# Kernel optimization log

Hardware: AMD Instinct MI355X
Metric: run time of the kernel (lower is better)

The kernel has to match this reference:

```python
import jax, jax.numpy as jnp
import numpy as np

H = 768          # hidden_size
NH = 12          # num heads
HD = H // NH     # head dim = 64
FF = 4 * H       # 3072
EPS = 1e-12


def _layer_norm(x, g, b):
    mu = jnp.mean(x, axis=-1, keepdims=True)
    var = jnp.var(x, axis=-1, keepdims=True)
    return (x - mu) * jax.lax.rsqrt(var + EPS) * g + b


def setup_inputs() -> dict:
    key = jax.random.key(0)
    ks = jax.random.split(key, 8)
    B, S = 4, 2048
    s = 0.02
    return {
        "x": jax.random.normal(ks[0], (B, S, H), dtype=jnp.float32),
        "w_qkv": jax.random.normal(ks[1], (H, 3 * H), dtype=jnp.float32) * s,
        "b_qkv": jnp.zeros((3 * H,), dtype=jnp.float32),
        "w_out": jax.random.normal(ks[2], (H, H), dtype=jnp.float32) * s,
        "b_out": jnp.zeros((H,), dtype=jnp.float32),
        "w_ff1": jax.random.normal(ks[3], (H, FF), dtype=jnp.float32) * s,
        "b_ff1": jnp.zeros((FF,), dtype=jnp.float32),
        "w_ff2": jax.random.normal(ks[4], (FF, H), dtype=jnp.float32) * s,
        "b_ff2": jnp.zeros((H,), dtype=jnp.float32),
        "g1": jnp.ones((H,), dtype=jnp.float32),
        "be1": jnp.zeros((H,), dtype=jnp.float32),
        "g2": jnp.ones((H,), dtype=jnp.float32),
        "be2": jnp.zeros((H,), dtype=jnp.float32),
    }


def reference(x, w_qkv, b_qkv, w_out, b_out, w_ff1, b_ff1, w_ff2, b_ff2, g1, be1, g2, be2):
    B, S, _ = x.shape
    qkv = x @ w_qkv + b_qkv                     # [B,S,3H]
    q, k, v = jnp.split(qkv, 3, axis=-1)
    # [B,S,H] -> [B,NH,S,HD]
    def heads(t):
        return t.reshape(B, S, NH, HD).transpose(0, 2, 1, 3)
    q, k, v = heads(q), heads(k), heads(v)
    scores = jnp.einsum("bhqd,bhkd->bhqk", q, k) / np.sqrt(HD).astype(np.float32)
    attn = jax.nn.softmax(scores, axis=-1)      # dropout is identity at inference
    ctx = jnp.einsum("bhqk,bhkd->bhqd", attn, v)
    ctx = ctx.transpose(0, 2, 1, 3).reshape(B, S, H)
    attn_out = ctx @ w_out + b_out
    x1 = _layer_norm(x + attn_out, g1, be1)
    h = jax.nn.gelu(x1 @ w_ff1 + b_ff1, approximate=False)  # torch exact gelu
    ffn = h @ w_ff2 + b_ff2
    return _layer_norm(x1 + ffn, g2, be2)
```

## Files before the change

### kernel.cpp

```cpp
#include <hip/hip_runtime.h>
#include <cstdint>
#include <cstddef>

typedef unsigned short u16;
typedef __attribute__((ext_vector_type(8))) short bf16x8;
typedef __attribute__((ext_vector_type(4))) float f32x4;
typedef __attribute__((ext_vector_type(16))) float f32x16;

__device__ __forceinline__ u16 f2b(float f) {
    union { float f; unsigned u; } un; un.f = f;
    unsigned r = un.u + 0x7fffu + ((un.u >> 16) & 1u);
    return (u16)(r >> 16);
}
__device__ __forceinline__ float b2f(u16 h) {
    union { unsigned u; float f; } un; un.u = ((unsigned)h) << 16;
    return un.f;
}
__device__ __forceinline__ float fast_exp2(float x) {
#if __has_builtin(__builtin_amdgcn_exp2f)
    return __builtin_amdgcn_exp2f(x);
#else
    return exp2f(x);
#endif
}
__device__ __forceinline__ float fast_rcp(float x) {
#if __has_builtin(__builtin_amdgcn_rcpf)
    return __builtin_amdgcn_rcpf(x);
#else
    return 1.f / x;
#endif
}
__device__ __forceinline__ float gelu_fast(float v) {
    const float s = fast_exp2(v * (2.30220842f + 0.10294324f * (v * v)));
    return v - v * fast_rcp(s + 1.f);
}

__device__ __forceinline__ void stage16(const u16* g, u16* l) {
    __builtin_amdgcn_global_load_lds(
        (const __attribute__((address_space(1))) void*)g,
        (__attribute__((address_space(3))) void*)l, 16, 0, 0);
}

__global__ __launch_bounds__(256)
void prep(const float* __restrict__ x, u16* __restrict__ xb,
          const float* __restrict__ wqkv, u16* __restrict__ wqkvT,
          const float* __restrict__ wout, u16* __restrict__ woutT,
          const float* __restrict__ wff1, u16* __restrict__ wff1T,
          const float* __restrict__ wff2, u16* __restrict__ wff2T) {
    __shared__ float t[32][33];
    const int tid = threadIdx.x;
    int bid = blockIdx.x;
    if (bid < 6144) {
        const int i = bid * 256 + tid;
        float4 v = ((const float4*)x)[i];
        ushort4 o;
        o.x = f2b(v.x); o.y = f2b(v.y); o.z = f2b(v.z); o.w = f2b(v.w);
        ((ushort4*)xb)[i] = o;
        return;
    }
    int tt = bid - 6144;
    const float* in; u16* out; int K, N, bx, by;
    if (tt < 1728)      { in = wqkv; out = wqkvT; K = 768;  N = 2304; bx = tt % 72; by = tt / 72; }
    else if ((tt -= 1728) < 576)  { in = wout; out = woutT; K = 768;  N = 768;  bx = tt % 24; by = tt / 24; }
    else if ((tt -= 576) < 2304)  { in = wff1; out = wff1T; K = 768;  N = 3072; bx = tt % 96; by = tt / 96; }
    else { tt -= 2304;    in = wff2; out = wff2T; K = 3072; N = 768;  bx = tt % 24; by = tt / 24; }
    const int n0 = bx * 32, k0 = by * 32;
    const int tx = tid & 31, ty = tid >> 5;
#pragma unroll
    for (int i = 0; i < 4; ++i)
        t[ty + i * 8][tx] = in[(size_t)(k0 + ty + i * 8) * N + n0 + tx];
    __syncthreads();
#pragma unroll
    for (int i = 0; i < 4; ++i)
        out[(size_t)(n0 + ty + i * 8) * K + k0 + tx] = f2b(t[tx][ty + i * 8]);
}

template <int EPI, int NTW>
__global__ __launch_bounds__(256, 3)
void gemm_bf16(const u16* __restrict__ A, const u16* __restrict__ BT,
               const float* __restrict__ bias,
               void* __restrict__ outp, u16* __restrict__ vt, int M, int N, int K) {
    __shared__ __align__(16) u16 Ash[128 * 64];
    __shared__ __align__(16) u16 Bsh[NTW * 64 * 64];
    const int m0 = blockIdx.y * 128, n0 = blockIdx.x * (NTW * 64);
    const int tid = threadIdx.x;
    const int w = tid >> 6, lane = tid & 63;
    const int l32 = lane & 31, half = lane >> 5;
    const int wm = (w >> 1) * 64, wn = (w & 1) * (NTW * 32);

    const int srow = lane >> 3;
    const int sgrp = (lane & 7) ^ (srow & 7);
    const int xr = l32 & 7;

    f32x16 acc[2][NTW];
#pragma unroll
    for (int i = 0; i < 2; ++i)
#pragma unroll
        for (int j = 0; j < NTW; ++j)
#pragma unroll
            for (int e = 0; e < 16; ++e) acc[i][j][e] = 0.f;

    for (int k0 = 0; k0 < K; k0 += 64) {
#pragma unroll
        for (int it = 0; it < 4; ++it) {
            const int c = it * 4 + w;
            const int r = c * 8 + srow;
            stage16(A + (size_t)(m0 + r) * K + k0 + sgrp * 8, &Ash[c * 512 + lane * 8]);
        }
#pragma unroll
        for (int it = 0; it < 2 * NTW; ++it) {
            const int c = it * 4 + w;
            const int r = c * 8 + srow;
            stage16(BT + (size_t)(n0 + r) * K + k0 + sgrp * 8, &Bsh[c * 512 + lane * 8]);
        }
        __syncthreads();

        if constexpr (NTW == 2) {
            bf16x8 af[2][4], bfr[2][4];
#pragma unroll
            for (int mt = 0; mt < 2; ++mt)
#pragma unroll
                for (int kc = 0; kc < 4; ++kc)
                    af[mt][kc] = *(const bf16x8*)&Ash[(wm + mt * 32 + l32) * 64 +
                                                      (((kc << 1) + half) ^ xr) * 8];
#pragma unroll
            for (int nt = 0; nt < 2; ++nt)
#pragma unroll
                for (int kc = 0; kc < 4; ++kc)
                    bfr[nt][kc] = *(const bf16x8*)&Bsh[(wn + nt * 32 + l32) * 64 +
                                                       (((kc << 1) + half) ^ xr) * 8];
#pragma unroll
            for (int mt = 0; mt < 2; ++mt)
#pragma unroll
                for (int nt = 0; nt < 2; ++nt)
#pragma unroll
                    for (int kc = 0; kc < 4; ++kc)
                        acc[mt][nt] = __builtin_amdgcn_mfma_f32_32x32x16_bf16(
                            af[mt][kc], bfr[nt][kc], acc[mt][nt], 0, 0, 0);
        } else {
#pragma unroll
            for (int kc = 0; kc < 4; ++kc) {
                const int ko = (((kc << 1) + half) ^ xr) * 8;
                bf16x8 a0 = *(const bf16x8*)&Ash[(wm + l32) * 64 + ko];
                bf16x8 a1 = *(const bf16x8*)&Ash[(wm + 32 + l32) * 64 + ko];
#pragma unroll
                for (int nt = 0; nt < NTW; ++nt) {
                    bf16x8 bv = *(const bf16x8*)&Bsh[(wn + nt * 32 + l32) * 64 + ko];
                    acc[0][nt] = __builtin_amdgcn_mfma_f32_32x32x16_bf16(
                        a0, bv, acc[0][nt], 0, 0, 0);
                    acc[1][nt] = __builtin_amdgcn_mfma_f32_32x32x16_bf16(
                        a1, bv, acc[1][nt], 0, 0, 0);
                }
            }
        }
        __syncthreads();
    }

    if (EPI == 3 && n0 >= 1536) {
#pragma unroll
        for (int mt = 0; mt < 2; ++mt) {
#pragma unroll
            for (int nt = 0; nt < NTW; ++nt) {
                const int col = n0 + wn + nt * 32 + l32;
                const int c = col - 1536;
                const int h = c >> 6, d = c & 63;
                const float bv = bias[col];
#pragma unroll
                for (int rq = 0; rq < 4; ++rq) {
                    const int row0 = m0 + wm + mt * 32 + rq * 8 + half * 4;
                    const int b = row0 >> 11, tok = row0 & 2047;
                    ushort4 o;
                    o.x = f2b(acc[mt][nt][rq * 4 + 0] + bv);
                    o.y = f2b(acc[mt][nt][rq * 4 + 1] + bv);
                    o.z = f2b(acc[mt][nt][rq * 4 + 2] + bv);
                    o.w = f2b(acc[mt][nt][rq * 4 + 3] + bv);
                    *(ushort4*)&vt[(size_t)(((b * 12 + h) << 6) + d) * 2048 + tok] = o;
                }
            }
        }
        return;
    }

#pragma unroll
    for (int mt = 0; mt < 2; ++mt) {
#pragma unroll
        for (int nt = 0; nt < NTW; ++nt) {
            const int col = n0 + wn + nt * 32 + l32;
            const float bv = bias[col];
#pragma unroll
            for (int reg = 0; reg < 16; ++reg) {
                const int row = m0 + wm + mt * 32 + (reg & 3) + 8 * (reg >> 2) + 4 * half;
                float v = acc[mt][nt][reg] + bv;
                if (EPI == 2)
                    v = gelu_fast(v);
                ((u16*)outp)[(size_t)row * N + col] = f2b(v);
            }
        }
    }
}

template <bool RESF32>
__global__ __launch_bounds__(256, 4)
void gemm_bf16_r64(const u16* __restrict__ A, const u16* __restrict__ BT,
                   const float* __restrict__ bias, const void* __restrict__ resid,
                   u16* __restrict__ outp, int M, int N, int K) {
    __shared__ __align__(16) u16 Ash[64 * 64];
    __shared__ __align__(16) u16 Bsh[128 * 64];
    const int m0 = blockIdx.y * 64, n0 = blockIdx.x * 128;
    const int tid = threadIdx.x;
    const int w = tid >> 6, lane = tid & 63;
    const int l32 = lane & 31, half = lane >> 5;
    const int wm = (w >> 1) * 32, wn = (w & 1) * 64;

    const int srow = lane >> 3;
    const int sgrp = (lane & 7) ^ (srow & 7);
    const int xr = l32 & 7;

    f32x16 acc[2];
#pragma unroll
    for (int j = 0; j < 2; ++j)
#pragma unroll
        for (int e = 0; e < 16; ++e) acc[j][e] = 0.f;

    for (int k0 = 0; k0 < K; k0 += 64) {
#pragma unroll
        for (int it = 0; it < 2; ++it) {
            const int c = it * 4 + w;
            const int r = c * 8 + srow;
            stage16(A + (size_t)(m0 + r) * K + k0 + sgrp * 8, &Ash[c * 512 + lane * 8]);
        }
#pragma unroll
        for (int it = 0; it < 4; ++it) {
            const int c = it * 4 + w;
            const int r = c * 8 + srow;
            stage16(BT + (size_t)(n0 + r) * K + k0 + sgrp * 8, &Bsh[c * 512 + lane * 8]);
        }
        __syncthreads();

        bf16x8 af[4], bfr[2][4];
#pragma unroll
        for (int kc = 0; kc < 4; ++kc)
            af[kc] = *(const bf16x8*)&Ash[(wm + l32) * 64 + (((kc << 1) + half) ^ xr) * 8];
#pragma unroll
        for (int nt = 0; nt < 2; ++nt)
#pragma unroll
            for (int kc = 0; kc < 4; ++kc)
                bfr[nt][kc] = *(const bf16x8*)&Bsh[(wn + nt * 32 + l32) * 64 +
                                                   (((kc << 1) + half) ^ xr) * 8];
#pragma unroll
        for (int nt = 0; nt < 2; ++nt)
#pragma unroll
            for (int kc = 0; kc < 4; ++kc)
                acc[nt] = __builtin_amdgcn_mfma_f32_32x32x16_bf16(
                    af[kc], bfr[nt][kc], acc[nt], 0, 0, 0);
        __syncthreads();
    }

#pragma unroll
    for (int nt = 0; nt < 2; ++nt) {
        const int col = n0 + wn + nt * 32 + l32;
        const float bv = bias[col];
#pragma unroll
        for (int reg = 0; reg < 16; ++reg) {
            const int row = m0 + wm + (reg & 3) + 8 * (reg >> 2) + 4 * half;
            const size_t idx = (size_t)row * N + col;
            const float rv = RESF32 ? ((const float*)resid)[idx]
                                    : b2f(((const u16*)resid)[idx]);
            outp[idx] = f2b(acc[nt][reg] + bv + rv);
        }
    }
}

__global__ __launch_bounds__(256, 3)
void attn_fused(const u16* __restrict__ qkv, const u16* __restrict__ vt,
                u16* __restrict__ ctx) {
    __shared__ __align__(16) u16 Ksh[2][64 * 64];
    __shared__ __align__(16) u16 Vsh[2][64 * 64];

    const int orig = blockIdx.x;
    const int swz = (orig & 7) * 96 + (orig >> 3);
    const int q0 = (swz & 15) * 128;
    const int bh = swz >> 4;
    const int h = bh % 12, b = bh / 12;

    const int tid = threadIdx.x;
    const int w = tid >> 6, lane = tid & 63;
    const int l32 = lane & 31, hi5 = lane >> 5;
    const int xr8 = l32 & 7;

    const int srow = lane >> 3;
    const int sgrp = (lane & 7) ^ (srow & 7);

    const u16* Qp = qkv + (size_t)b * 2048 * 2304 + h * 64;
    const u16* Kp = Qp + 768;
    const u16* Vtp = vt + ((size_t)(b * 12 + h) << 6) * 2048;

    bf16x8 qf[4];
#pragma unroll
    for (int ks = 0; ks < 4; ++ks)
        qf[ks] = *(const bf16x8*)(Qp +
            (size_t)(q0 + w * 32 + l32) * 2304 + ks * 16 + hi5 * 8);
    asm volatile("s_waitcnt vmcnt(0)" ::: "memory");
    __builtin_amdgcn_sched_barrier(0);

    f32x16 oacc[2];
#pragma unroll
    for (int dt = 0; dt < 2; ++dt)
#pragma unroll
        for (int e = 0; e < 16; ++e) oacc[dt][e] = 0.f;
    float ls0 = 0.f, ls1 = 0.f, ls2 = 0.f, ls3 = 0.f;

    constexpr float SCALE = 0.18033688011112042f;

    auto stage_kv = [&](int buf, int ktt) {
#pragma unroll
        for (int it = 0; it < 2; ++it) {
            const int c = it * 4 + w;
            const int r = c * 8 + srow;
            stage16(Kp + (size_t)(ktt + r) * 2304 + sgrp * 8,
                    &Ksh[buf][c * 512 + lane * 8]);
        }
#pragma unroll
        for (int it = 0; it < 2; ++it) {
            const int c = it * 4 + w;
            const int r = c * 8 + srow;
            stage16(Vtp + (size_t)r * 2048 + ktt + sgrp * 8,
                    &Vsh[buf][c * 512 + lane * 8]);
        }
    };

    stage_kv(0, 0);

    for (int t = 0; t < 32; ++t) {
        const int cur = t & 1;
        if (t < 31) {
            stage_kv(cur ^ 1, (t + 1) * 64);
            asm volatile("s_waitcnt vmcnt(4)" ::: "memory");
        } else {
            asm volatile("s_waitcnt vmcnt(0)" ::: "memory");
        }
        __builtin_amdgcn_sched_barrier(0);
        __builtin_amdgcn_s_barrier();

        f32x16 sacc[2];
#pragma unroll
        for (int nt = 0; nt < 2; ++nt)
#pragma unroll
            for (int e = 0; e < 16; ++e) sacc[nt][e] = 0.f;

        __builtin_amdgcn_s_setprio(1);
#pragma unroll
        for (int nt = 0; nt < 2; ++nt)
#pragma unroll
            for (int ks = 0; ks < 4; ++ks) {
                bf16x8 kfr = *(const bf16x8*)&Ksh[cur][(nt * 32 + l32) * 64 +
                                                      (((ks << 1) + hi5) ^ xr8) * 8];
                sacc[nt] = __builtin_amdgcn_mfma_f32_32x32x16_bf16(
                    kfr, qf[ks], sacc[nt], 0, 0, 0);
            }
        __builtin_amdgcn_s_setprio(0);

#pragma unroll
        for (int nt = 0; nt < 2; ++nt) {
#pragma unroll
            for (int e = 0; e < 16; ++e)
                sacc[nt][e] = fast_exp2(sacc[nt][e] * SCALE);
            ls0 += sacc[nt][0] + sacc[nt][1];
            ls1 += sacc[nt][2] + sacc[nt][3];
            ls2 += sacc[nt][4] + sacc[nt][5];
            ls3 += sacc[nt][6] + sacc[nt][7];
            ls0 += sacc[nt][8] + sacc[nt][9];
            ls1 += sacc[nt][10] + sacc[nt][11];
            ls2 += sacc[nt][12] + sacc[nt][13];
            ls3 += sacc[nt][14] + sacc[nt][15];
        }

        __builtin_amdgcn_s_setprio(1);
#pragma unroll
        for (int nt = 0; nt < 2; ++nt) {
#pragma unroll
            for (int kh = 0; kh < 2; ++kh) {
                const int rb = kh * 8;
                unsigned c01, c23, c45, c67;
                asm("v_cvt_pk_bf16_f32 %0, %1, %2"
                    : "=v"(c01) : "v"(sacc[nt][rb + 0]), "v"(sacc[nt][rb + 1]));
                asm("v_cvt_pk_bf16_f32 %0, %1, %2"
                    : "=v"(c23) : "v"(sacc[nt][rb + 2]), "v"(sacc[nt][rb + 3]));
                asm("v_cvt_pk_bf16_f32 %0, %1, %2"
                    : "=v"(c45) : "v"(sacc[nt][rb + 4]), "v"(sacc[nt][rb + 5]));
                asm("v_cvt_pk_bf16_f32 %0, %1, %2"
                    : "=v"(c67) : "v"(sacc[nt][rb + 6]), "v"(sacc[nt][rb + 7]));
                asm("v_permlane32_swap_b32 %0, %1" : "+v"(c01), "+v"(c45));
                asm("v_permlane32_swap_b32 %0, %1" : "+v"(c23), "+v"(c67));
                union { unsigned u[4]; bf16x8 v; } pf;
                pf.u[0] = c01; pf.u[1] = c23; pf.u[2] = c45; pf.u[3] = c67;
#pragma unroll
                for (int dt = 0; dt < 2; ++dt) {
                    bf16x8 vfr = *(const bf16x8*)&Vsh[cur][(dt * 32 + l32) * 64 +
                        (((nt << 2) + (kh << 1) + hi5) ^ xr8) * 8];
                    oacc[dt] = __builtin_amdgcn_mfma_f32_32x32x16_bf16(
                        pf.v, vfr, oacc[dt], 0, 0, 0);
                }
            }
        }
        __builtin_amdgcn_s_setprio(0);
        __builtin_amdgcn_s_barrier();
    }

    float lsum = (ls0 + ls1) + (ls2 + ls3);
    lsum += __shfl_xor(lsum, 32);
    const float linv = 1.f / lsum;

    float scv[16];
#pragma unroll
    for (int reg = 0; reg < 16; ++reg) {
        const int q_r = (reg & 3) + 8 * (reg >> 2) + 4 * hi5;
        scv[reg] = __shfl(linv, q_r);
    }

#pragma unroll
    for (int dt = 0; dt < 2; ++dt)
#pragma unroll
        for (int reg = 0; reg < 16; ++reg) {
            const int q_r = (reg & 3) + 8 * (reg >> 2) + 4 * hi5;
            const int row = q0 + w * 32 + q_r;
            ctx[(size_t)(b * 2048 + row) * 768 + h * 64 + dt * 32 + l32] =
                f2b(oacc[dt][reg] * scv[reg]);
        }
}

template <bool OUTF32>
__global__ __launch_bounds__(256)
void layernorm_k(const u16* __restrict__ y, const float* __restrict__ g,
                 const float* __restrict__ be, float* __restrict__ outf,
                 u16* __restrict__ outb) {
    const int row = blockIdx.x;
    const int tid = threadIdx.x;
    const u16* yr = y + (size_t)row * 768;
    float v[3], s = 0.f, s2 = 0.f;
#pragma unroll
    for (int i = 0; i < 3; ++i) {
        float x = b2f(yr[tid + i * 256]);
        v[i] = x; s += x; s2 += x * x;
    }
#pragma unroll
    for (int off = 32; off >= 1; off >>= 1) {
        s += __shfl_xor(s, off);
        s2 += __shfl_xor(s2, off);
    }
    __shared__ float red[2][4];
    const int w = tid >> 6;
    if ((tid & 63) == 0) { red[0][w] = s; red[1][w] = s2; }
    __syncthreads();
    s = red[0][0] + red[0][1] + red[0][2] + red[0][3];
    s2 = red[1][0] + red[1][1] + red[1][2] + red[1][3];
    const float mu = s * (1.f / 768.f);
    const float var = s2 * (1.f / 768.f) - mu * mu;
    const float rs = rsqrtf(var + 1e-12f);
#pragma unroll
    for (int i = 0; i < 3; ++i) {
        const int c = tid + i * 256;
        const float o = (v[i] - mu) * rs * g[c] + be[c];
        if (OUTF32) outf[(size_t)row * 768 + c] = o;
        else        outb[(size_t)row * 768 + c] = f2b(o);
    }
}

extern "C" void kernel_launch(void* const* d_in, const int* in_sizes, int n_in,
                              void* d_out, int out_size, void* d_ws, size_t ws_size,
                              hipStream_t stream) {
    const float* x    = (const float*)d_in[0];
    const float* wqkv = (const float*)d_in[1];
    const float* bqkv = (const float*)d_in[2];
    const float* wout = (const float*)d_in[3];
    const float* bout = (const float*)d_in[4];
    const float* wff1 = (const float*)d_in[5];
    const float* bff1 = (const float*)d_in[6];
    const float* wff2 = (const float*)d_in[7];
    const float* bff2 = (const float*)d_in[8];
    const float* g1   = (const float*)d_in[9];
    const float* be1  = (const float*)d_in[10];
    const float* g2   = (const float*)d_in[11];
    const float* be2  = (const float*)d_in[12];

    char* ws = (char*)d_ws;
    constexpr size_t o_xb    = 0;
    constexpr size_t o_wqkvT = o_xb    + (size_t)8192 * 768 * 2;
    constexpr size_t o_woutT = o_wqkvT + (size_t)2304 * 768 * 2;
    constexpr size_t o_wff1T = o_woutT + (size_t)768 * 768 * 2;
    constexpr size_t o_wff2T = o_wff1T + (size_t)3072 * 768 * 2;
    constexpr size_t o_qkv   = o_wff2T + (size_t)768 * 3072 * 2;
    constexpr size_t o_ctx   = o_qkv   + (size_t)8192 * 2304 * 2;
    constexpr size_t o_y     = o_ctx   + (size_t)8192 * 768 * 2;
    constexpr size_t o_x1b   = o_y     + (size_t)8192 * 768 * 2;
    constexpr size_t o_vt    = o_x1b;
    constexpr size_t o_h     = o_qkv;

    u16*   xb    = (u16*)(ws + o_xb);
    u16*   wqkvT = (u16*)(ws + o_wqkvT);
    u16*   woutT = (u16*)(ws + o_woutT);
    u16*   wff1T = (u16*)(ws + o_wff1T);
    u16*   wff2T = (u16*)(ws + o_wff2T);
    u16*   qkvb  = (u16*)(ws + o_qkv);
    u16*   ctxb  = (u16*)(ws + o_ctx);
    u16*   yb    = (u16*)(ws + o_y);
    u16*   x1b   = (u16*)(ws + o_x1b);
    u16*   hb    = (u16*)(ws + o_h);
    u16*   vt    = (u16*)(ws + o_vt);

    prep<<<13056, 256, 0, stream>>>(x, xb, wqkv, wqkvT, wout, woutT,
                                    wff1, wff1T, wff2, wff2T);

    gemm_bf16<3, 3><<<dim3(2304 / 192, 8192 / 128), 256, 0, stream>>>(
        xb, wqkvT, bqkv, qkvb, vt, 8192, 2304, 768);

    attn_fused<<<768, 256, 0, stream>>>(qkvb, vt, ctxb);

    gemm_bf16_r64<true><<<dim3(768 / 128, 8192 / 64), 256, 0, stream>>>(
        ctxb, woutT, bout, x, yb, 8192, 768, 768);

    layernorm_k<false><<<8192, 256, 0, stream>>>(yb, g1, be1, nullptr, x1b);

    gemm_bf16<2, 2><<<dim3(3072 / 128, 8192 / 128), 256, 0, stream>>>(
        x1b, wff1T, bff1, hb, nullptr, 8192, 3072, 768);

    gemm_bf16_r64<false><<<dim3(768 / 128, 8192 / 64), 256, 0, stream>>>(
        hb, wff2T, bff2, x1b, yb, 8192, 768, 3072);

    layernorm_k<true><<<8192, 256, 0, stream>>>(yb, g2, be2, (float*)d_out, nullptr);
}
```

Before: 367.6 us.

## Load K/V fragments directly from global memory in attention, fold scale into QKV GEMM

Removes the LDS double-buffered staging of K and V tiles in the attention kernel, along with its barriers and waitcnts. Each wave now reads its MFMA K and V fragments straight from global memory, relying on L2/L1 for the reuse across waves. The softmax scale (log2e/sqrt(d)) moves into the QKV GEMM epilogue, which scales the Q columns, so the attention loop drops a multiply per score. The risk is more global/L1 traffic and exposed load latency, since there is no prefetch or software pipelining.

```diff
diff --git a/kernel.cpp b/kernel.cpp
--- a/kernel.cpp
+++ b/kernel.cpp
@@ -193,6 +193,8 @@
                 float v = acc[mt][nt][reg] + bv;
                 if (EPI == 2)
                     v = gelu_fast(v);
+                if (EPI == 3 && col < 768)
+                    v *= 0.18033688011112042f;
                 ((u16*)outp)[(size_t)row * N + col] = f2b(v);
             }
         }
@@ -274,9 +276,6 @@
 __global__ __launch_bounds__(256, 3)
 void attn_fused(const u16* __restrict__ qkv, const u16* __restrict__ vt,
                 u16* __restrict__ ctx) {
-    __shared__ __align__(16) u16 Ksh[2][64 * 64];
-    __shared__ __align__(16) u16 Vsh[2][64 * 64];
-
     const int orig = blockIdx.x;
     const int swz = (orig & 7) * 96 + (orig >> 3);
     const int q0 = (swz & 15) * 128;
@@ -286,10 +285,6 @@
     const int tid = threadIdx.x;
     const int w = tid >> 6, lane = tid & 63;
     const int l32 = lane & 31, hi5 = lane >> 5;
-    const int xr8 = l32 & 7;
-
-    const int srow = lane >> 3;
-    const int sgrp = (lane & 7) ^ (srow & 7);
 
     const u16* Qp = qkv + (size_t)b * 2048 * 2304 + h * 64;
     const u16* Kp = Qp + 768;
@@ -300,8 +295,6 @@
     for (int ks = 0; ks < 4; ++ks)
         qf[ks] = *(const bf16x8*)(Qp +
             (size_t)(q0 + w * 32 + l32) * 2304 + ks * 16 + hi5 * 8);
-    asm volatile("s_waitcnt vmcnt(0)" ::: "memory");
-    __builtin_amdgcn_sched_barrier(0);
 
     f32x16 oacc[2];
 #pragma unroll
@@ -310,101 +303,58 @@
         for (int e = 0; e < 16; ++e) oacc[dt][e] = 0.f;
     float ls0 = 0.f, ls1 = 0.f, ls2 = 0.f, ls3 = 0.f;
 
-    constexpr float SCALE = 0.18033688011112042f;
-
-    auto stage_kv = [&](int buf, int ktt) {
-#pragma unroll
-        for (int it = 0; it < 2; ++it) {
-            const int c = it * 4 + w;
-            const int r = c * 8 + srow;
-            stage16(Kp + (size_t)(ktt + r) * 2304 + sgrp * 8,
-                    &Ksh[buf][c * 512 + lane * 8]);
-        }
-#pragma unroll
-        for (int it = 0; it < 2; ++it) {
-            const int c = it * 4 + w;
-            const int r = c * 8 + srow;
-            stage16(Vtp + (size_t)r * 2048 + ktt + sgrp * 8,
-                    &Vsh[buf][c * 512 + lane * 8]);
-        }
-    };
-
-    stage_kv(0, 0);
-
-    for (int t = 0; t < 32; ++t) {
-        const int cur = t & 1;
-        if (t < 31) {
-            stage_kv(cur ^ 1, (t + 1) * 64);
-            asm volatile("s_waitcnt vmcnt(4)" ::: "memory");
-        } else {
-            asm volatile("s_waitcnt vmcnt(0)" ::: "memory");
-        }
-        __builtin_amdgcn_sched_barrier(0);
-        __builtin_amdgcn_s_barrier();
-
-        f32x16 sacc[2];
-#pragma unroll
-        for (int nt = 0; nt < 2; ++nt)
-#pragma unroll
-            for (int e = 0; e < 16; ++e) sacc[nt][e] = 0.f;
-
-        __builtin_amdgcn_s_setprio(1);
-#pragma unroll
-        for (int nt = 0; nt < 2; ++nt)
-#pragma unroll
-            for (int ks = 0; ks < 4; ++ks) {
-                bf16x8 kfr = *(const bf16x8*)&Ksh[cur][(nt * 32 + l32) * 64 +
-                                                      (((ks << 1) + hi5) ^ xr8) * 8];
-                sacc[nt] = __builtin_amdgcn_mfma_f32_32x32x16_bf16(
-                    kfr, qf[ks], sacc[nt], 0, 0, 0);
-            }
-        __builtin_amdgcn_s_setprio(0);
-
+    const u16* Krow = Kp + (size_t)l32 * 2304 + hi5 * 8;
+    const u16* Vrow = Vtp + (size_t)l32 * 2048 + hi5 * 8;
+
+    for (int kt = 0; kt < 2048; kt += 64) {
 #pragma unroll
         for (int nt = 0; nt < 2; ++nt) {
-#pragma unroll
-            for (int e = 0; e < 16; ++e)
-                sacc[nt][e] = fast_exp2(sacc[nt][e] * SCALE);
-            ls0 += sacc[nt][0] + sacc[nt][1];
-            ls1 += sacc[nt][2] + sacc[nt][3];
-            ls2 += sacc[nt][4] + sacc[nt][5];
-            ls3 += sacc[nt][6] + sacc[nt][7];
-            ls0 += sacc[nt][8] + sacc[nt][9];
-            ls1 += sacc[nt][10] + sacc[nt][11];
-            ls2 += sacc[nt][12] + sacc[nt][13];
-            ls3 += sacc[nt][14] + sacc[nt][15];
-        }
-
-        __builtin_amdgcn_s_setprio(1);
-#pragma unroll
-        for (int nt = 0; nt < 2; ++nt) {
+            const u16* kbase = Krow + (size_t)(kt + nt * 32) * 2304;
+            bf16x8 kfr[4];
+#pragma unroll
+            for (int ks = 0; ks < 4; ++ks)
+                kfr[ks] = *(const bf16x8*)(kbase + ks * 16);
+
+            f32x16 sacc;
+#pragma unroll
+            for (int e = 0; e < 16; ++e) sacc[e] = 0.f;
+#pragma unroll
+            for (int ks = 0; ks < 4; ++ks)
+                sacc = __builtin_amdgcn_mfma_f32_32x32x16_bf16(
+                    kfr[ks], qf[ks], sacc, 0, 0, 0);
+
+#pragma unroll
+            for (int e = 0; e < 16; ++e) sacc[e] = fast_exp2(sacc[e]);
+            ls0 += (sacc[0] + sacc[1]) + (sacc[8] + sacc[9]);
+            ls1 += (sacc[2] + sacc[3]) + (sacc[10] + sacc[11]);
+            ls2 += (sacc[4] + sacc[5]) + (sacc[12] + sacc[13]);
+            ls3 += (sacc[6] + sacc[7]) + (sacc[14] + sacc[15]);
+
 #pragma unroll
             for (int kh = 0; kh < 2; ++kh) {
                 const int rb = kh * 8;
                 unsigned c01, c23, c45, c67;
                 asm("v_cvt_pk_bf16_f32 %0, %1, %2"
-                    : "=v"(c01) : "v"(sacc[nt][rb + 0]), "v"(sacc[nt][rb + 1]));
+                    : "=v"(c01) : "v"(sacc[rb + 0]), "v"(sacc[rb + 1]));
                 asm("v_cvt_pk_bf16_f32 %0, %1, %2"
-                    : "=v"(c23) : "v"(sacc[nt][rb + 2]), "v"(sacc[nt][rb + 3]));
+                    : "=v"(c23) : "v"(sacc[rb + 2]), "v"(sacc[rb + 3]));
                 asm("v_cvt_pk_bf16_f32 %0, %1, %2"
-                    : "=v"(c45) : "v"(sacc[nt][rb + 4]), "v"(sacc[nt][rb + 5]));
+                    : "=v"(c45) : "v"(sacc[rb + 4]), "v"(sacc[rb + 5]));
                 asm("v_cvt_pk_bf16_f32 %0, %1, %2"
-                    : "=v"(c67) : "v"(sacc[nt][rb + 6]), "v"(sacc[nt][rb + 7]));
+                    : "=v"(c67) : "v"(sacc[rb + 6]), "v"(sacc[rb + 7]));
                 asm("v_permlane32_swap_b32 %0, %1" : "+v"(c01), "+v"(c45));
                 asm("v_permlane32_swap_b32 %0, %1" : "+v"(c23), "+v"(c67));
                 union { unsigned u[4]; bf16x8 v; } pf;
                 pf.u[0] = c01; pf.u[1] = c23; pf.u[2] = c45; pf.u[3] = c67;
 #pragma unroll
                 for (int dt = 0; dt < 2; ++dt) {
-                    bf16x8 vfr = *(const bf16x8*)&Vsh[cur][(dt * 32 + l32) * 64 +
-                        (((nt << 2) + (kh << 1) + hi5) ^ xr8) * 8];
+                    bf16x8 vfr = *(const bf16x8*)(Vrow +
+                        (size_t)dt * 32 * 2048 + kt + nt * 32 + kh * 16);
                     oacc[dt] = __builtin_amdgcn_mfma_f32_32x32x16_bf16(
                         pf.v, vfr, oacc[dt], 0, 0, 0);
                 }
             }
         }
-        __builtin_amdgcn_s_setprio(0);
-        __builtin_amdgcn_s_barrier();
     }
 
     float lsum = (ls0 + ls1) + (ls2 + ls3);
```

Measured after the change: 485.5 us. +32.1%, slower.
